# Performance work log

Hardware: AMD Instinct MI355X
Metric: run time of the kernel (lower is better)

## Reference

```python
import jax, jax.numpy as jnp
import numpy as np

HIDDEN_DIM = 256
NLAT, NLON = 64, 128
BATCH, N_STATIONS = 2, 1024


def _grid_coords():
    lat = jnp.linspace(-90.0, 90.0, NLAT)
    lon = jnp.linspace(-180.0, 180.0, NLON)
    lat_mesh, lon_mesh = jnp.meshgrid(lat, lon, indexing='ij')
    return lat_mesh.reshape(-1), lon_mesh.reshape(-1)  # (n_grid,)


def setup_inputs() -> dict:
    key = jax.random.key(0)
    k1, k2, k3, k4, k5, k6 = jax.random.split(key, 6)
    station_features = jax.random.normal(k1, (BATCH, N_STATIONS, HIDDEN_DIM), dtype=jnp.float32)
    station_coords = jax.random.normal(k2, (BATCH, N_STATIONS, 3), dtype=jnp.float32)
    mask = jnp.ones((BATCH, N_STATIONS), dtype=jnp.float32)
    # distance_mlp params: Linear(3,32) -> GELU -> Linear(32,1) -> Softplus
    W1 = jax.random.normal(k3, (3, 32), dtype=jnp.float32) * (1.0 / np.sqrt(3.0))
    b1 = jax.random.normal(k4, (32,), dtype=jnp.float32) * 0.02
    W2 = jax.random.normal(k5, (32, 1), dtype=jnp.float32) * (1.0 / np.sqrt(32.0))
    b2 = jax.random.normal(k6, (1,), dtype=jnp.float32) * 0.02
    return {"station_features": station_features, "station_coords": station_coords,
            "mask": mask, "W1": W1, "b1": b1, "W2": W2, "b2": b2}


def reference(station_features, station_coords, mask, W1, b1, W2, b2):
    lat_grid, lon_grid = _grid_coords()  # (G,)
    station_lat = station_coords[:, :, 0]  # (B,S)
    station_lon = station_coords[:, :, 1]
    dlat = station_lat[:, :, None] - lat_grid[None, None, :]  # (B,S,G)
    dlon = station_lon[:, :, None] - lon_grid[None, None, :]
    dist = jnp.sqrt(dlat**2 + dlon**2 + 1e-6)
    dist_features = jnp.stack([dist, dlat, dlon], axis=-1)  # (B,S,G,3)
    h = jax.nn.gelu(dist_features @ W1 + b1, approximate=False)  # (B,S,G,32)
    weights = jax.nn.softplus((h @ W2 + b2)[..., 0])  # (B,S,G)
    weights = weights * mask[:, :, None]
    weights = jax.nn.softmax(weights, axis=1)  # over stations
    grid = jnp.einsum('bsg,bsd->bgd', weights, station_features)
    grid = grid.reshape(station_features.shape[0], NLAT, NLON, HIDDEN_DIM)
    return jnp.transpose(grid, (0, 3, 1, 2))  # (B, D, nlat, nlon)
```

## Files before the change

### kernel.cpp

```cpp
#include <hip/hip_runtime.h>
#include <math.h>

#define NLAT 64
#define NLON 128
#define HID  256
#define NSTA 1024
#define TG   16
#define SC   256
#define NCHUNK (NSTA / SC)
#define NGRP 32
#define TABN 4096
#define TABW 4.5f

#define LOG2E 1.4426950408889634f
#define LN2   0.69314718055994531f

typedef float f32x4 __attribute__((ext_vector_type(4)));
typedef _Float16 f16x8 __attribute__((ext_vector_type(8)));

__device__ __forceinline__ float gelu_ref(float x) {
    const float p  = 0.3275911f;
    const float a1 = 0.254829592f, a2 = -0.284496736f, a3 = 1.421413741f,
                a4 = -1.453152027f, a5 = 1.061405429f;
    float z  = x * 0.70710678118654752f;
    float az = fabsf(z);
    float t  = __builtin_amdgcn_rcpf(fmaf(p, az, 1.0f));
    float poly = fmaf(fmaf(fmaf(fmaf(a5, t, a4), t, a3), t, a2), t, a1) * t;
    float e  = __builtin_amdgcn_exp2f(az * az * -LOG2E);
    float r  = fmaf(-poly, e, 1.0f);
    float erfz = copysignf(r, z);
    float hx = 0.5f * x;
    return fmaf(hx, erfz, hx);
}

__global__ __launch_bounds__(256)
void cvt_kernel(const float* __restrict__ feats, _Float16* __restrict__ fhi,
                _Float16* __restrict__ flo) {
    __shared__ float tile[64][68];
    const int blk = blockIdx.x;
    const int b  = blk >> 6;
    const int st = (blk >> 2) & 15;
    const int dt = blk & 3;
    {
        const int dq = threadIdx.x & 15;
        const int sr = threadIdx.x >> 4;
#pragma unroll
        for (int k = 0; k < 4; ++k) {
            int s = k * 16 + sr;
            float4 vv = *(const float4*)
                &feats[((size_t)(b * NSTA + st * 64 + s)) * HID + dt * 64 + dq * 4];
            *(float4*)&tile[s][dq * 4] = vv;
        }
    }
    __syncthreads();
    const int d  = threadIdx.x >> 2;
    const int sg = threadIdx.x & 3;
    f16x8 h8[2], l8[2];
#pragma unroll
    for (int k = 0; k < 16; ++k) {
        float v = tile[sg * 16 + k][d];
        _Float16 h = (_Float16)v;
        h8[k >> 3][k & 7] = h;
        l8[k >> 3][k & 7] = (_Float16)(v - (float)h);
    }
    const size_t o = ((size_t)(b * HID + dt * 64 + d)) * NSTA + st * 64 + sg * 16;
    *(f16x8*)&fhi[o]     = h8[0];
    *(f16x8*)&fhi[o + 8] = h8[1];
    *(f16x8*)&flo[o]     = l8[0];
    *(f16x8*)&flo[o + 8] = l8[1];
}

__global__ __launch_bounds__(512, 8)
void s2g_kernel(const float* __restrict__ coords,
                const float* __restrict__ maskp,
                const float* __restrict__ W1,
                const float* __restrict__ b1,
                const float* __restrict__ W2,
                const float* __restrict__ b2p,
                const _Float16* __restrict__ fhi,
                const _Float16* __restrict__ flo,
                float* __restrict__ out)
{
    __shared__ __align__(16) float gtab[TABN];
    __shared__ __align__(16) f16x8 fragAh[512];
    __shared__ __align__(16) float slat[SC], slon[SC], smask[SC];
    __shared__ float4 wpack[32];
    __shared__ float w2s[32];
    __shared__ __align__(16) float maxbuf[NGRP * TG], psum[NGRP * TG];
    __shared__ __align__(16) float mS[TG], lS[TG], alphaS[TG];

    const int tid  = threadIdx.x;
    const int blk  = blockIdx.x & 511;
    const int b    = blockIdx.x >> 9;
    const int lat  = blk >> 3;
    const int lon0 = (blk & 7) * TG;

    const float latv = -90.0f + (180.0f / 63.0f) * (float)lat;

    const float TH = 2.0f * TABW / (float)TABN;
#pragma unroll
    for (int k = tid; k < TABN; k += 512) {
        float x = -TABW + ((float)k + 0.5f) * TH;
        gtab[k] = gelu_ref(x) - fmaxf(x, 0.0f);
    }
    if (tid < 32) {
        wpack[tid] = make_float4(W1[tid], W1[32 + tid], W1[64 + tid], b1[tid]);
        w2s[tid]   = W2[tid];
        if (tid < TG) { mS[tid] = -1.0e30f; lS[tid] = 0.0f; }
    }
    const float b2 = b2p[0];

    const int gA   = tid & (TG - 1);
    const int sgrp = tid >> 4;
    const float lonvA = -180.0f + (360.0f / 127.0f) * (float)(lon0 + gA);

    const int lane = tid & 63;
    const int wv   = tid >> 6;
    const int kc0  = (wv >> 2) * 4;
    const int dsel = (wv & 3) * 64;

    f32x4 acc[4];
#pragma unroll
    for (int t = 0; t < 4; ++t) acc[t] = (f32x4){0.0f, 0.0f, 0.0f, 0.0f};

    const float* cbase = coords + (size_t)b * NSTA * 3;
    const float* mbase = maskp  + (size_t)b * NSTA;
    const _Float16* fhb = fhi + (size_t)b * HID * NSTA;
    const _Float16* flb = flo + (size_t)b * HID * NSTA;

    const float ISCALE = (float)TABN / (2.0f * TABW);
    const float IOFF   = (float)TABN * 0.5f;

    for (int c = 0; c < NCHUNK; ++c) {
        const int s0 = c * SC;
        __syncthreads();
        if (tid < SC) {
            slat[tid]  = cbase[(size_t)(s0 + tid) * 3 + 0];
            slon[tid]  = cbase[(size_t)(s0 + tid) * 3 + 1];
            smask[tid] = mbase[s0 + tid];
        }
        __syncthreads();

        float dist[8], dlat[8], dlon[8], v[8];
#pragma unroll
        for (int i = 0; i < 8; ++i) {
            int s = sgrp * 8 + i;
            float dla = slat[s] - latv;
            float dlo = slon[s] - lonvA;
            dlat[i] = dla;
            dlon[i] = dlo;
            dist[i] = sqrtf(fmaf(dla, dla, fmaf(dlo, dlo, 1e-6f)));
            v[i] = b2;
        }
#pragma unroll 2
        for (int j = 0; j < 32; ++j) {
            float4 wj = wpack[j];
            float  w2 = w2s[j];
#pragma unroll
            for (int i = 0; i < 8; ++i) {
                float pre = fmaf(wj.x, dist[i], fmaf(wj.y, dlat[i], fmaf(wj.z, dlon[i], wj.w)));
                float cl  = fminf(fmaxf(pre, -TABW), 4.4999f);
                int  idx  = (int)fmaf(cl, ISCALE, IOFF);
                float ge  = fmaxf(pre, 0.0f) + gtab[idx];
                v[i] = fmaf(w2, ge, v[i]);
            }
        }
        float lmax = -3.0e38f;
#pragma unroll
        for (int i = 0; i < 8; ++i) {
            int s = sgrp * 8 + i;
            float x  = v[i];
            float ax = fabsf(x);
            float e  = __builtin_amdgcn_exp2f(-ax * LOG2E);
            float sp = fmaxf(x, 0.0f) + __builtin_amdgcn_logf(1.0f + e) * LN2;
            v[i] = sp * smask[s];
            lmax = fmaxf(lmax, v[i]);
        }
        maxbuf[sgrp * TG + gA] = lmax;
        __syncthreads();

        if (tid < TG) {
            float cm = maxbuf[tid];
#pragma unroll
            for (int k = 1; k < NGRP; ++k) cm = fmaxf(cm, maxbuf[k * TG + tid]);
            float mold = mS[tid];
            float mnew = fmaxf(mold, cm);
            alphaS[tid] = __builtin_amdgcn_exp2f((mold - mnew) * LOG2E);
            mS[tid] = mnew;
        }
        __syncthreads();

        {
            float m  = mS[gA];
            float ps = 0.0f;
            f16x8 fh;
#pragma unroll
            for (int i = 0; i < 8; ++i) {
                float p = __builtin_amdgcn_exp2f((v[i] - m) * LOG2E);
                fh[i] = (_Float16)p;
                ps += p;
            }
            fragAh[((sgrp >> 2) << 6) + (((sgrp & 3) << 4) | gA)] = fh;
            psum[sgrp * TG + gA] = ps;
        }
        __syncthreads();

        if (tid < TG) {
            float t = 0.0f;
#pragma unroll
            for (int k = 0; k < NGRP; ++k) t += psum[k * TG + tid];
            lS[tid] = lS[tid] * alphaS[tid] + t;
        }

        {
            const f32x4 al = *(const f32x4*)&alphaS[(lane >> 4) * 4];
#pragma unroll
            for (int t = 0; t < 4; ++t) acc[t] = acc[t] * al;

            const int srow = (lane >> 4) * 8;
            const int dbase = dsel + (lane & 15);
#pragma unroll
            for (int kc = 0; kc < 4; ++kc) {
                f16x8 a = fragAh[((kc0 + kc) << 6) + lane];
#pragma unroll
                for (int t = 0; t < 4; ++t) {
                    const size_t off = (size_t)(dbase + t * 16) * NSTA +
                                       s0 + (kc0 + kc) * 32 + srow;
                    f16x8 bh = *(const f16x8*)(fhb + off);
                    f16x8 bl = *(const f16x8*)(flb + off);
                    acc[t] = __builtin_amdgcn_mfma_f32_16x16x32_f16(a, bh, acc[t], 0, 0, 0);
                    acc[t] = __builtin_amdgcn_mfma_f32_16x16x32_f16(a, bl, acc[t], 0, 0, 0);
                }
            }
        }
    }
    __syncthreads();

    {
        f32x4* red = reinterpret_cast<f32x4*>(gtab);
        if (wv >= 4) {
#pragma unroll
            for (int t = 0; t < 4; ++t) red[(((wv & 3) * 4 + t) << 6) + lane] = acc[t];
        }
        __syncthreads();
        if (wv < 4) {
            const float4 l4 = *(const float4*)&lS[(lane >> 4) * 4];
            const float4 rl = make_float4(1.0f / l4.x, 1.0f / l4.y, 1.0f / l4.z, 1.0f / l4.w);
            const int m0 = (lane >> 4) * 4;
            const size_t gbase = (size_t)lat * NLON + lon0 + m0;
#pragma unroll
            for (int t = 0; t < 4; ++t) {
                f32x4 s = acc[t] + red[((wv * 4 + t) << 6) + lane];
                const int d = dsel + t * 16 + (lane & 15);
                float4 o;
                o.x = s.x * rl.x;
                o.y = s.y * rl.y;
                o.z = s.z * rl.z;
                o.w = s.w * rl.w;
                *reinterpret_cast<float4*>(out + ((size_t)(b * HID + d)) * (NLAT * NLON) + gbase) = o;
            }
        }
    }
}

extern "C" void kernel_launch(void* const* d_in, const int* in_sizes, int n_in,
                              void* d_out, int out_size, void* d_ws, size_t ws_size,
                              hipStream_t stream) {
    const float* feats  = (const float*)d_in[0];
    const float* coords = (const float*)d_in[1];
    const float* maskp  = (const float*)d_in[2];
    const float* W1     = (const float*)d_in[3];
    const float* b1     = (const float*)d_in[4];
    const float* W2     = (const float*)d_in[5];
    const float* b2     = (const float*)d_in[6];
    float* out          = (float*)d_out;

    _Float16* fhi = (_Float16*)d_ws;
    _Float16* flo = fhi + (size_t)2 * HID * NSTA;

    hipLaunchKernelGGL(cvt_kernel, dim3(128), dim3(256), 0, stream, feats, fhi, flo);
    hipLaunchKernelGGL(s2g_kernel, dim3(1024), dim3(512), 0, stream,
                       coords, maskp, W1, b1, W2, b2, fhi, flo, out);
}
```

Baseline: 274.8 us.

## Halve grid tile to 8 points, shrink GELU table with linear interpolation

Each block now covers 8 grid longitudes with 256 threads instead of 16 with 512, launching twice as many blocks. The MFMA rows for the missing 8 grid points are zero-padded, so each wave runs all 8 k-chunks itself and the cross-wave reduction at the end goes away. The GELU lookup table drops from 4096 to 513 entries and uses linear interpolation, which cuts table build time and LDS use but adds a second LDS read per lookup. Half of the MFMA work is wasted on padding, and each block now reads the full feature stream, which doubles global/L2 traffic for features.

Result: slower. 364.3 us (+32.6%).

```diff
diff --git a/kernel.cpp b/kernel.cpp
--- a/kernel.cpp
+++ b/kernel.cpp
@@ -5,11 +5,11 @@
 #define NLON 128
 #define HID  256
 #define NSTA 1024
-#define TG   16
+#define TG   8
 #define SC   256
 #define NCHUNK (NSTA / SC)
 #define NGRP 32
-#define TABN 4096
+#define TABN 512
 #define TABW 4.5f
 
 #define LOG2E 1.4426950408889634f
@@ -70,7 +70,7 @@
     *(f16x8*)&flo[o + 8] = l8[1];
 }
 
-__global__ __launch_bounds__(512, 8)
+__global__ __launch_bounds__(256, 8)
 void s2g_kernel(const float* __restrict__ coords,
                 const float* __restrict__ maskp,
                 const float* __restrict__ W1,
@@ -81,43 +81,44 @@
                 const _Float16* __restrict__ flo,
                 float* __restrict__ out)
 {
-    __shared__ __align__(16) float gtab[TABN];
+    __shared__ __align__(8) float gtab[TABN + 1];
     __shared__ __align__(16) f16x8 fragAh[512];
     __shared__ __align__(16) float slat[SC], slon[SC], smask[SC];
     __shared__ float4 wpack[32];
     __shared__ float w2s[32];
     __shared__ __align__(16) float maxbuf[NGRP * TG], psum[NGRP * TG];
-    __shared__ __align__(16) float mS[TG], lS[TG], alphaS[TG];
+    __shared__ __align__(16) float mS[16], lS[16], alphaS[16];
 
     const int tid  = threadIdx.x;
-    const int blk  = blockIdx.x & 511;
-    const int b    = blockIdx.x >> 9;
-    const int lat  = blk >> 3;
-    const int lon0 = (blk & 7) * TG;
+    const int blk  = blockIdx.x & 1023;
+    const int b    = blockIdx.x >> 10;
+    const int lat  = blk >> 4;
+    const int lon0 = (blk & 15) * TG;
 
     const float latv = -90.0f + (180.0f / 63.0f) * (float)lat;
 
     const float TH = 2.0f * TABW / (float)TABN;
 #pragma unroll
-    for (int k = tid; k < TABN; k += 512) {
-        float x = -TABW + ((float)k + 0.5f) * TH;
+    for (int k = tid; k < TABN + 1; k += 256) {
+        float x = -TABW + (float)k * TH;
         gtab[k] = gelu_ref(x) - fmaxf(x, 0.0f);
     }
+    fragAh[tid]       = (f16x8)(_Float16)0.0f;
+    fragAh[tid + 256] = (f16x8)(_Float16)0.0f;
     if (tid < 32) {
         wpack[tid] = make_float4(W1[tid], W1[32 + tid], W1[64 + tid], b1[tid]);
         w2s[tid]   = W2[tid];
-        if (tid < TG) { mS[tid] = -1.0e30f; lS[tid] = 0.0f; }
+        if (tid < 16) { mS[tid] = -1.0e30f; lS[tid] = 0.0f; alphaS[tid] = 1.0f; }
     }
     const float b2 = b2p[0];
 
     const int gA   = tid & (TG - 1);
-    const int sgrp = tid >> 4;
+    const int sgrp = tid >> 3;
     const float lonvA = -180.0f + (360.0f / 127.0f) * (float)(lon0 + gA);
 
     const int lane = tid & 63;
     const int wv   = tid >> 6;
-    const int kc0  = (wv >> 2) * 4;
-    const int dsel = (wv & 3) * 64;
+    const int dsel = wv * 64;
 
     f32x4 acc[4];
 #pragma unroll
@@ -159,9 +160,14 @@
 #pragma unroll
             for (int i = 0; i < 8; ++i) {
                 float pre = fmaf(wj.x, dist[i], fmaf(wj.y, dlat[i], fmaf(wj.z, dlon[i], wj.w)));
-                float cl  = fminf(fmaxf(pre, -TABW), 4.4999f);
-                int  idx  = (int)fmaf(cl, ISCALE, IOFF);
-                float ge  = fmaxf(pre, 0.0f) + gtab[idx];
+                float cl  = fminf(fmaxf(pre, -TABW), 4.49999f);
+                float u   = fmaf(cl, ISCALE, IOFF);
+                float fu  = floorf(u);
+                float fr  = u - fu;
+                int   idx = (int)fu;
+                float g0  = gtab[idx];
+                float g1  = gtab[idx + 1];
+                float ge  = fmaxf(pre, 0.0f) + fmaf(fr, g1 - g0, g0);
                 v[i] = fmaf(w2, ge, v[i]);
             }
         }
@@ -187,6 +193,8 @@
             float mnew = fmaxf(mold, cm);
             alphaS[tid] = __builtin_amdgcn_exp2f((mold - mnew) * LOG2E);
             mS[tid] = mnew;
+        } else if (tid < 16) {
+            alphaS[tid] = 1.0f;
         }
         __syncthreads();
 
@@ -220,12 +228,12 @@
             const int srow = (lane >> 4) * 8;
             const int dbase = dsel + (lane & 15);
 #pragma unroll
-            for (int kc = 0; kc < 4; ++kc) {
-                f16x8 a = fragAh[((kc0 + kc) << 6) + lane];
+            for (int kc = 0; kc < 8; ++kc) {
+                f16x8 a = fragAh[(kc << 6) + lane];
 #pragma unroll
                 for (int t = 0; t < 4; ++t) {
                     const size_t off = (size_t)(dbase + t * 16) * NSTA +
-                                       s0 + (kc0 + kc) * 32 + srow;
+                                       s0 + kc * 32 + srow;
                     f16x8 bh = *(const f16x8*)(fhb + off);
                     f16x8 bl = *(const f16x8*)(flb + off);
                     acc[t] = __builtin_amdgcn_mfma_f32_16x16x32_f16(a, bh, acc[t], 0, 0, 0);
@@ -236,29 +244,20 @@
     }
     __syncthreads();
 
-    {
-        f32x4* red = reinterpret_cast<f32x4*>(gtab);
-        if (wv >= 4) {
-#pragma unroll
-            for (int t = 0; t < 4; ++t) red[(((wv & 3) * 4 + t) << 6) + lane] = acc[t];
-        }
-        __syncthreads();
-        if (wv < 4) {
-            const float4 l4 = *(const float4*)&lS[(lane >> 4) * 4];
-            const float4 rl = make_float4(1.0f / l4.x, 1.0f / l4.y, 1.0f / l4.z, 1.0f / l4.w);
-            const int m0 = (lane >> 4) * 4;
-            const size_t gbase = (size_t)lat * NLON + lon0 + m0;
-#pragma unroll
-            for (int t = 0; t < 4; ++t) {
-                f32x4 s = acc[t] + red[((wv * 4 + t) << 6) + lane];
-                const int d = dsel + t * 16 + (lane & 15);
-                float4 o;
-                o.x = s.x * rl.x;
-                o.y = s.y * rl.y;
-                o.z = s.z * rl.z;
-                o.w = s.w * rl.w;
-                *reinterpret_cast<float4*>(out + ((size_t)(b * HID + d)) * (NLAT * NLON) + gbase) = o;
-            }
+    if (lane < 32) {
+        const float4 l4 = *(const float4*)&lS[(lane >> 4) * 4];
+        const float4 rl = make_float4(1.0f / l4.x, 1.0f / l4.y, 1.0f / l4.z, 1.0f / l4.w);
+        const int m0 = (lane >> 4) * 4;
+        const size_t gbase = (size_t)lat * NLON + lon0 + m0;
+#pragma unroll
+        for (int t = 0; t < 4; ++t) {
+            const int d = dsel + t * 16 + (lane & 15);
+            float4 o;
+            o.x = acc[t].x * rl.x;
+            o.y = acc[t].y * rl.y;
+            o.z = acc[t].z * rl.z;
+            o.w = acc[t].w * rl.w;
+            *reinterpret_cast<float4*>(out + ((size_t)(b * HID + d)) * (NLAT * NLON) + gbase) = o;
         }
     }
 }
@@ -279,6 +278,6 @@
     _Float16* flo = fhi + (size_t)2 * HID * NSTA;
 
     hipLaunchKernelGGL(cvt_kernel, dim3(128), dim3(256), 0, stream, feats, fhi, flo);
-    hipLaunchKernelGGL(s2g_kernel, dim3(1024), dim3(512), 0, stream,
+    hipLaunchKernelGGL(s2g_kernel, dim3(2048), dim3(256), 0, stream,
                        coords, maskp, W1, b1, W2, b2, fhi, flo, out);
 }
```

## Split into score and GEMM kernels with interval-bounded GELU hidden-unit pruning

Applied to the files above, without the earlier changes.

Replaces the fused online-softmax kernel with three stages: feature conversion, a score kernel that computes full per-grid-point softmax weights (fp16) over all stations, and a separate MFMA GEMM kernel. In the score kernel, interval bounds on the station coordinate range classify each hidden unit as linear (its GELU folded into an affine term), negligible (dropped), or nonlinear (evaluated with the table), which aims to cut MLP work per station. The cost is a large fp16 weight matrix written to and reread from global memory, plus fp16 rounding of the normalized weights instead of the unnormalized ones. The dropped and linear units are approximations bounded only by the chosen margin.

Result: slower. 333.1 us (+21.2%).

```diff
diff --git a/kernel.cpp b/kernel.cpp
--- a/kernel.cpp
+++ b/kernel.cpp
@@ -5,12 +5,10 @@
 #define NLON 128
 #define HID  256
 #define NSTA 1024
-#define TG   16
-#define SC   256
-#define NCHUNK (NSTA / SC)
-#define NGRP 32
+#define NG   8192
 #define TABN 4096
 #define TABW 4.5f
+#define CLS_MARGIN 4.55f
 
 #define LOG2E 1.4426950408889634f
 #define LN2   0.69314718055994531f
@@ -70,195 +68,215 @@
     *(f16x8*)&flo[o + 8] = l8[1];
 }
 
-__global__ __launch_bounds__(512, 8)
-void s2g_kernel(const float* __restrict__ coords,
-                const float* __restrict__ maskp,
-                const float* __restrict__ W1,
-                const float* __restrict__ b1,
-                const float* __restrict__ W2,
-                const float* __restrict__ b2p,
-                const _Float16* __restrict__ fhi,
-                const _Float16* __restrict__ flo,
-                float* __restrict__ out)
+__global__ __launch_bounds__(256, 4)
+void score_kernel(const float* __restrict__ coords,
+                  const float* __restrict__ maskp,
+                  const float* __restrict__ W1,
+                  const float* __restrict__ b1,
+                  const float* __restrict__ W2,
+                  const float* __restrict__ b2p,
+                  _Float16* __restrict__ wn)
 {
-    __shared__ __align__(16) float gtab[TABN];
-    __shared__ __align__(16) f16x8 fragAh[512];
-    __shared__ __align__(16) float slat[SC], slon[SC], smask[SC];
+    __shared__ __align__(8) float gtab[TABN];
+    __shared__ __align__(16) float slat[NSTA], slon[NSTA], smask[NSTA];
     __shared__ float4 wpack[32];
     __shared__ float w2s[32];
-    __shared__ __align__(16) float maxbuf[NGRP * TG], psum[NGRP * TG];
-    __shared__ __align__(16) float mS[TG], lS[TG], alphaS[TG];
+    __shared__ int nlidxS[4][32];
 
     const int tid  = threadIdx.x;
-    const int blk  = blockIdx.x & 511;
     const int b    = blockIdx.x >> 9;
-    const int lat  = blk >> 3;
-    const int lon0 = (blk & 7) * TG;
-
-    const float latv = -90.0f + (180.0f / 63.0f) * (float)lat;
+    const int g0   = (blockIdx.x & 511) * 16;
+    const int lane = tid & 63;
+    const int wv   = tid >> 6;
 
     const float TH = 2.0f * TABW / (float)TABN;
-#pragma unroll
-    for (int k = tid; k < TABN; k += 512) {
+    for (int k = tid; k < TABN; k += 256) {
         float x = -TABW + ((float)k + 0.5f) * TH;
         gtab[k] = gelu_ref(x) - fmaxf(x, 0.0f);
     }
     if (tid < 32) {
         wpack[tid] = make_float4(W1[tid], W1[32 + tid], W1[64 + tid], b1[tid]);
         w2s[tid]   = W2[tid];
-        if (tid < TG) { mS[tid] = -1.0e30f; lS[tid] = 0.0f; }
     }
     const float b2 = b2p[0];
-
-    const int gA   = tid & (TG - 1);
-    const int sgrp = tid >> 4;
-    const float lonvA = -180.0f + (360.0f / 127.0f) * (float)(lon0 + gA);
-
-    const int lane = tid & 63;
-    const int wv   = tid >> 6;
-    const int kc0  = (wv >> 2) * 4;
-    const int dsel = (wv & 3) * 64;
-
-    f32x4 acc[4];
-#pragma unroll
-    for (int t = 0; t < 4; ++t) acc[t] = (f32x4){0.0f, 0.0f, 0.0f, 0.0f};
-
-    const float* cbase = coords + (size_t)b * NSTA * 3;
-    const float* mbase = maskp  + (size_t)b * NSTA;
-    const _Float16* fhb = fhi + (size_t)b * HID * NSTA;
-    const _Float16* flb = flo + (size_t)b * HID * NSTA;
+    {
+        const float* cb = coords + (size_t)b * NSTA * 3;
+        const float* mb = maskp  + (size_t)b * NSTA;
+        for (int k = tid; k < NSTA; k += 256) {
+            slat[k]  = cb[k * 3 + 0];
+            slon[k]  = cb[k * 3 + 1];
+            smask[k] = mb[k];
+        }
+    }
+    __syncthreads();
+
+    float lamin = 1.0e30f, lamax = -1.0e30f, lomin = 1.0e30f, lomax = -1.0e30f;
+#pragma unroll 4
+    for (int i = 0; i < 16; ++i) {
+        float la = slat[i * 64 + lane];
+        float lo = slon[i * 64 + lane];
+        lamin = fminf(lamin, la); lamax = fmaxf(lamax, la);
+        lomin = fminf(lomin, lo); lomax = fmaxf(lomax, lo);
+    }
+#pragma unroll
+    for (int off = 32; off >= 1; off >>= 1) {
+        lamin = fminf(lamin, __shfl_xor(lamin, off));
+        lamax = fmaxf(lamax, __shfl_xor(lamax, off));
+        lomin = fminf(lomin, __shfl_xor(lomin, off));
+        lomax = fmaxf(lomax, __shfl_xor(lomax, off));
+    }
 
     const float ISCALE = (float)TABN / (2.0f * TABW);
     const float IOFF   = (float)TABN * 0.5f;
 
-    for (int c = 0; c < NCHUNK; ++c) {
-        const int s0 = c * SC;
-        __syncthreads();
-        if (tid < SC) {
-            slat[tid]  = cbase[(size_t)(s0 + tid) * 3 + 0];
-            slon[tid]  = cbase[(size_t)(s0 + tid) * 3 + 1];
-            smask[tid] = mbase[s0 + tid];
-        }
-        __syncthreads();
-
-        float dist[8], dlat[8], dlon[8], v[8];
-#pragma unroll
-        for (int i = 0; i < 8; ++i) {
-            int s = sgrp * 8 + i;
-            float dla = slat[s] - latv;
-            float dlo = slon[s] - lonvA;
-            dlat[i] = dla;
-            dlon[i] = dlo;
-            dist[i] = sqrtf(fmaf(dla, dla, fmaf(dlo, dlo, 1e-6f)));
-            v[i] = b2;
-        }
-#pragma unroll 2
-        for (int j = 0; j < 32; ++j) {
-            float4 wj = wpack[j];
+    for (int it = 0; it < 4; ++it) {
+        const int g = g0 + wv * 4 + it;
+        const float latv = -90.0f + (180.0f / 63.0f) * (float)(g >> 7);
+        const float lonv = -180.0f + (360.0f / 127.0f) * (float)(g & 127);
+
+        const int jj = lane & 31;
+        float4 wj = wpack[jj];
+        float w2j = w2s[jj];
+        float dla_lo = lamin - latv, dla_hi = lamax - latv;
+        float dlo_lo = lomin - lonv, dlo_hi = lomax - lonv;
+        float a2a = dla_lo * dla_lo, a2b = dla_hi * dla_hi;
+        float a2lo = (dla_lo > 0.0f) ? a2a : ((dla_hi < 0.0f) ? a2b : 0.0f);
+        float a2hi = fmaxf(a2a, a2b);
+        float b2a = dlo_lo * dlo_lo, b2b = dlo_hi * dlo_hi;
+        float b2lo = (dlo_lo > 0.0f) ? b2a : ((dlo_hi < 0.0f) ? b2b : 0.0f);
+        float b2hi = fmaxf(b2a, b2b);
+        float d_lo = sqrtf(a2lo + b2lo + 1e-6f);
+        float d_hi = sqrtf(a2hi + b2hi + 1e-6f);
+        float pxl = fminf(wj.x * d_lo, wj.x * d_hi), pxh = fmaxf(wj.x * d_lo, wj.x * d_hi);
+        float pyl = fminf(wj.y * dla_lo, wj.y * dla_hi), pyh = fmaxf(wj.y * dla_lo, wj.y * dla_hi);
+        float pzl = fminf(wj.z * dlo_lo, wj.z * dlo_hi), pzh = fmaxf(wj.z * dlo_lo, wj.z * dlo_hi);
+        float plo = wj.w + pxl + pyl + pzl;
+        float phi = wj.w + pxh + pyh + pzh;
+        bool isLin = (plo > CLS_MARGIN);
+        bool isNL  = (!isLin) && (phi >= -CLS_MARGIN);
+        float cx = isLin ? w2j * wj.x : 0.0f;
+        float cy = isLin ? w2j * wj.y : 0.0f;
+        float cz = isLin ? w2j * wj.z : 0.0f;
+        float cc = isLin ? w2j * wj.w : 0.0f;
+#pragma unroll
+        for (int off = 16; off >= 1; off >>= 1) {
+            cx += __shfl_xor(cx, off);
+            cy += __shfl_xor(cy, off);
+            cz += __shfl_xor(cz, off);
+            cc += __shfl_xor(cc, off);
+        }
+        unsigned long long mb64 = __ballot(isNL);
+        unsigned mlow = (unsigned)(mb64 & 0xffffffffull);
+        const int nn = __popc(mlow);
+        if (lane < 32 && isNL) {
+            int pos = __popc(mlow & ((1u << lane) - 1u));
+            nlidxS[wv][pos] = jj;
+        }
+
+        float dist[16], dla[16], vsc[16];
+        const float vb = b2 + cc;
+#pragma unroll 4
+        for (int i = 0; i < 16; ++i) {
+            int s = i * 64 + lane;
+            float a = slat[s] - latv;
+            float o = slon[s] - lonv;
+            float dd = sqrtf(fmaf(a, a, fmaf(o, o, 1e-6f)));
+            dla[i] = a;
+            dist[i] = dd;
+            vsc[i] = fmaf(cx, dd, fmaf(cy, a, fmaf(cz, o, vb)));
+        }
+        for (int k = 0; k < nn; ++k) {
+            int j = nlidxS[wv][k];
+            float4 w = wpack[j];
             float  w2 = w2s[j];
-#pragma unroll
-            for (int i = 0; i < 8; ++i) {
-                float pre = fmaf(wj.x, dist[i], fmaf(wj.y, dlat[i], fmaf(wj.z, dlon[i], wj.w)));
-                float cl  = fminf(fmaxf(pre, -TABW), 4.4999f);
+#pragma unroll 4
+            for (int i = 0; i < 16; ++i) {
+                float o = slon[i * 64 + lane] - lonv;
+                float pre = fmaf(w.x, dist[i], fmaf(w.y, dla[i], fmaf(w.z, o, w.w)));
+                float cl  = fminf(fmaxf(pre, -TABW), 4.49945f);
                 int  idx  = (int)fmaf(cl, ISCALE, IOFF);
-                float ge  = fmaxf(pre, 0.0f) + gtab[idx];
-                v[i] = fmaf(w2, ge, v[i]);
+                vsc[i] = fmaf(w2, fmaxf(pre, 0.0f) + gtab[idx], vsc[i]);
             }
         }
-        float lmax = -3.0e38f;
-#pragma unroll
-        for (int i = 0; i < 8; ++i) {
-            int s = sgrp * 8 + i;
-            float x  = v[i];
+        float mx = -3.0e38f;
+#pragma unroll 4
+        for (int i = 0; i < 16; ++i) {
+            int s = i * 64 + lane;
+            float x  = vsc[i];
             float ax = fabsf(x);
             float e  = __builtin_amdgcn_exp2f(-ax * LOG2E);
             float sp = fmaxf(x, 0.0f) + __builtin_amdgcn_logf(1.0f + e) * LN2;
-            v[i] = sp * smask[s];
-            lmax = fmaxf(lmax, v[i]);
-        }
-        maxbuf[sgrp * TG + gA] = lmax;
-        __syncthreads();
-
-        if (tid < TG) {
-            float cm = maxbuf[tid];
-#pragma unroll
-            for (int k = 1; k < NGRP; ++k) cm = fmaxf(cm, maxbuf[k * TG + tid]);
-            float mold = mS[tid];
-            float mnew = fmaxf(mold, cm);
-            alphaS[tid] = __builtin_amdgcn_exp2f((mold - mnew) * LOG2E);
-            mS[tid] = mnew;
-        }
-        __syncthreads();
-
-        {
-            float m  = mS[gA];
-            float ps = 0.0f;
-            f16x8 fh;
-#pragma unroll
-            for (int i = 0; i < 8; ++i) {
-                float p = __builtin_amdgcn_exp2f((v[i] - m) * LOG2E);
-                fh[i] = (_Float16)p;
-                ps += p;
-            }
-            fragAh[((sgrp >> 2) << 6) + (((sgrp & 3) << 4) | gA)] = fh;
-            psum[sgrp * TG + gA] = ps;
-        }
-        __syncthreads();
-
-        if (tid < TG) {
-            float t = 0.0f;
-#pragma unroll
-            for (int k = 0; k < NGRP; ++k) t += psum[k * TG + tid];
-            lS[tid] = lS[tid] * alphaS[tid] + t;
-        }
-
-        {
-            const f32x4 al = *(const f32x4*)&alphaS[(lane >> 4) * 4];
-#pragma unroll
-            for (int t = 0; t < 4; ++t) acc[t] = acc[t] * al;
-
-            const int srow = (lane >> 4) * 8;
-            const int dbase = dsel + (lane & 15);
-#pragma unroll
-            for (int kc = 0; kc < 4; ++kc) {
-                f16x8 a = fragAh[((kc0 + kc) << 6) + lane];
-#pragma unroll
-                for (int t = 0; t < 4; ++t) {
-                    const size_t off = (size_t)(dbase + t * 16) * NSTA +
-                                       s0 + (kc0 + kc) * 32 + srow;
-                    f16x8 bh = *(const f16x8*)(fhb + off);
-                    f16x8 bl = *(const f16x8*)(flb + off);
-                    acc[t] = __builtin_amdgcn_mfma_f32_16x16x32_f16(a, bh, acc[t], 0, 0, 0);
-                    acc[t] = __builtin_amdgcn_mfma_f32_16x16x32_f16(a, bl, acc[t], 0, 0, 0);
-                }
-            }
-        }
-    }
-    __syncthreads();
-
-    {
-        f32x4* red = reinterpret_cast<f32x4*>(gtab);
-        if (wv >= 4) {
-#pragma unroll
-            for (int t = 0; t < 4; ++t) red[(((wv & 3) * 4 + t) << 6) + lane] = acc[t];
-        }
-        __syncthreads();
-        if (wv < 4) {
-            const float4 l4 = *(const float4*)&lS[(lane >> 4) * 4];
-            const float4 rl = make_float4(1.0f / l4.x, 1.0f / l4.y, 1.0f / l4.z, 1.0f / l4.w);
-            const int m0 = (lane >> 4) * 4;
-            const size_t gbase = (size_t)lat * NLON + lon0 + m0;
-#pragma unroll
-            for (int t = 0; t < 4; ++t) {
-                f32x4 s = acc[t] + red[((wv * 4 + t) << 6) + lane];
-                const int d = dsel + t * 16 + (lane & 15);
-                float4 o;
-                o.x = s.x * rl.x;
-                o.y = s.y * rl.y;
-                o.z = s.z * rl.z;
-                o.w = s.w * rl.w;
-                *reinterpret_cast<float4*>(out + ((size_t)(b * HID + d)) * (NLAT * NLON) + gbase) = o;
-            }
+            vsc[i] = sp * smask[s];
+            mx = fmaxf(mx, vsc[i]);
+        }
+#pragma unroll
+        for (int off = 32; off >= 1; off >>= 1) mx = fmaxf(mx, __shfl_xor(mx, off));
+        float sum = 0.0f;
+#pragma unroll 4
+        for (int i = 0; i < 16; ++i) {
+            float p = __builtin_amdgcn_exp2f((vsc[i] - mx) * LOG2E);
+            vsc[i] = p;
+            sum += p;
+        }
+#pragma unroll
+        for (int off = 32; off >= 1; off >>= 1) sum += __shfl_xor(sum, off);
+        float rl = __builtin_amdgcn_rcpf(sum);
+        _Float16* wp = wn + ((size_t)(b * NG + g)) * NSTA;
+#pragma unroll 4
+        for (int i = 0; i < 16; ++i)
+            wp[i * 64 + lane] = (_Float16)(vsc[i] * rl);
+    }
+}
+
+__global__ __launch_bounds__(256)
+void gemm_kernel(const _Float16* __restrict__ wn,
+                 const _Float16* __restrict__ fhi,
+                 const _Float16* __restrict__ flo,
+                 float* __restrict__ out)
+{
+    const int blk  = blockIdx.x;
+    const int b    = blk >> 8;
+    const int gt   = (blk & 255) * 32;
+    const int lane = threadIdx.x & 63;
+    const int wv   = threadIdx.x >> 6;
+    const int dsel = wv * 64;
+    const int quad = lane >> 4;
+    const int nidx = lane & 15;
+
+    f32x4 acc[2][4];
+#pragma unroll
+    for (int m = 0; m < 2; ++m)
+#pragma unroll
+        for (int t = 0; t < 4; ++t) acc[m][t] = (f32x4){0.0f, 0.0f, 0.0f, 0.0f};
+
+    const _Float16* wb  = wn  + ((size_t)(b * NG + gt)) * NSTA;
+    const _Float16* fhb = fhi + (size_t)b * HID * NSTA;
+    const _Float16* flb = flo + (size_t)b * HID * NSTA;
+
+#pragma unroll 4
+    for (int kc = 0; kc < 32; ++kc) {
+        const int soff = kc * 32 + quad * 8;
+        f16x8 a0 = *(const f16x8*)(wb + (size_t)nidx * NSTA + soff);
+        f16x8 a1 = *(const f16x8*)(wb + (size_t)(nidx + 16) * NSTA + soff);
+#pragma unroll
+        for (int t = 0; t < 4; ++t) {
+            const size_t fo = (size_t)(dsel + t * 16 + nidx) * NSTA + soff;
+            f16x8 bh = *(const f16x8*)(fhb + fo);
+            f16x8 bl = *(const f16x8*)(flb + fo);
+            acc[0][t] = __builtin_amdgcn_mfma_f32_16x16x32_f16(a0, bh, acc[0][t], 0, 0, 0);
+            acc[0][t] = __builtin_amdgcn_mfma_f32_16x16x32_f16(a0, bl, acc[0][t], 0, 0, 0);
+            acc[1][t] = __builtin_amdgcn_mfma_f32_16x16x32_f16(a1, bh, acc[1][t], 0, 0, 0);
+            acc[1][t] = __builtin_amdgcn_mfma_f32_16x16x32_f16(a1, bl, acc[1][t], 0, 0, 0);
+        }
+    }
+
+#pragma unroll
+    for (int m = 0; m < 2; ++m) {
+#pragma unroll
+        for (int t = 0; t < 4; ++t) {
+            const int d = dsel + t * 16 + nidx;
+            float* op = out + ((size_t)(b * HID + d)) * NG + gt + m * 16 + quad * 4;
+            *reinterpret_cast<float4*>(op) = *(float4*)&acc[m][t];
         }
     }
 }
@@ -277,8 +295,11 @@
 
     _Float16* fhi = (_Float16*)d_ws;
     _Float16* flo = fhi + (size_t)2 * HID * NSTA;
-
-    hipLaunchKernelGGL(cvt_kernel, dim3(128), dim3(256), 0, stream, feats, fhi, flo);
-    hipLaunchKernelGGL(s2g_kernel, dim3(1024), dim3(512), 0, stream,
-                       coords, maskp, W1, b1, W2, b2, fhi, flo, out);
-}
+    _Float16* wn  = flo + (size_t)2 * HID * NSTA;
+
+    hipLaunchKernelGGL(cvt_kernel,   dim3(128),  dim3(256), 0, stream, feats, fhi, flo);
+    hipLaunchKernelGGL(score_kernel, dim3(1024), dim3(256), 0, stream,
+                       coords, maskp, W1, b1, W2, b2, wn);
+    hipLaunchKernelGGL(gemm_kernel,  dim3(512),  dim3(256), 0, stream,
+                       wn, fhi, flo, out);
+}
```
